# Optimization experiments

Hardware: AMD Instinct MI355X
Metric: run time of the kernel (lower is better)

The kernel has to match this reference:

```python
import jax, jax.numpy as jnp
import numpy as np

N = 100000      # nodes
E = 1600000     # edges
IN = 128        # in_dim
PE = 16         # pe_dim
HID = 128       # hid_dim
LAT = 64        # lat_dim
K = 4           # Chebyshev order


def setup_inputs() -> dict:
    key = jax.random.key(0)
    ks = jax.random.split(key, 12)
    f_in = IN + PE
    return {
        "x": jax.random.normal(ks[0], (N, IN), dtype=jnp.float32),
        "edge_index": jax.random.randint(ks[1], (2, E), 0, N, dtype=jnp.int32),
        "lap_pe": jax.random.normal(ks[2], (N, PE), dtype=jnp.float32),
        "edge_weight": jax.random.uniform(ks[3], (E,), dtype=jnp.float32),
        "W1": jax.random.normal(ks[4], (K, f_in, HID), dtype=jnp.float32) / np.sqrt(f_in),
        "b1": jnp.zeros((HID,), dtype=jnp.float32),
        "W2": jax.random.normal(ks[5], (K, HID, HID), dtype=jnp.float32) / np.sqrt(HID),
        "b2": jnp.zeros((HID,), dtype=jnp.float32),
        "W_mu": jax.random.normal(ks[6], (HID, LAT), dtype=jnp.float32) / np.sqrt(HID),
        "b_mu": jnp.zeros((LAT,), dtype=jnp.float32),
        "W_lv": jax.random.normal(ks[7], (HID, LAT), dtype=jnp.float32) / np.sqrt(HID),
        "b_lv": jnp.zeros((LAT,), dtype=jnp.float32),
    }


def _propagate(h, src, dst, w_hat):
    # (L_hat h)_i = sum_{(j->i)} w_hat_e * h_j   (one SpMM hop)
    return jax.ops.segment_sum(w_hat[:, None] * h[src], dst, num_segments=N)


def _cheb_conv(h, W, b, src, dst, w_hat):
    # PyG ChebConv recurrence: T0 = h, T1 = L_hat h, T_k = 2 L_hat T_{k-1} - T_{k-2}
    out = h @ W[0]
    tx0, tx1 = h, _propagate(h, src, dst, w_hat)
    out = out + tx1 @ W[1]
    for k in range(2, K):
        tx2 = 2.0 * _propagate(tx1, src, dst, w_hat) - tx0
        out = out + tx2 @ W[k]
        tx0, tx1 = tx1, tx2
    return out + b


def reference(x, edge_index, lap_pe, edge_weight, W1, b1, W2, b2, W_mu, b_mu, W_lv, b_lv):
    h = jnp.concatenate([x, lap_pe], axis=1)  # [N, IN+PE]
    src, dst = edge_index[0], edge_index[1]
    # ChebConv removes self loops before building the Laplacian -> zero their weight
    w = jnp.where(src == dst, 0.0, edge_weight)
    deg = jax.ops.segment_sum(w, src, num_segments=N)
    dinv = jnp.where(deg > 0, 1.0 / jnp.sqrt(deg), 0.0)
    # scaled Laplacian with lambda_max=2: L_hat = L - I = -D^{-1/2} A D^{-1/2}
    w_hat = -dinv[src] * w * dinv[dst]
    h = jax.nn.relu(_cheb_conv(h, W1, b1, src, dst, w_hat))
    h = jax.nn.relu(_cheb_conv(h, W2, b2, src, dst, w_hat))
    # scatter_mean with all-zero index == global mean pooling -> [1, HID]
    g = jnp.mean(h, axis=0, keepdims=True)
    return g @ W_mu + b_mu, g @ W_lv + b_lv
```

## Files before the change

### kernel.cpp

```cpp
#include <hip/hip_runtime.h>
#include <hip/hip_bf16.h>

#define IN_DIM 128
#define PE_DIM 16
#define F_IN 144
#define HID 128
#define LAT 64
#define K_CHEB 4

typedef unsigned int uint;
typedef unsigned short ushort;
typedef unsigned char uchar;
typedef __attribute__((ext_vector_type(8))) short short8;
typedef __attribute__((ext_vector_type(4))) float floatx4;
typedef __attribute__((ext_vector_type(2))) float floatx2;

__device__ __forceinline__ ushort f2bf(float f) {
    uint u = __float_as_uint(f);
    uint r = (u + 0x7FFFu + ((u >> 16) & 1u)) >> 16;
    return (ushort)r;
}
__device__ __forceinline__ uint bf_pack(float lo, float hi) {
    return (uint)f2bf(lo) | ((uint)f2bf(hi) << 16);
}

template<bool HI>
__device__ __forceinline__ floatx2 fp8x2_f32(uint v) {
    return __builtin_amdgcn_cvt_pk_f32_fp8((int)v, HI);
}
template<bool HI>
__device__ __forceinline__ uint f32_fp8x2(float a, float b, uint old) {
    return (uint)__builtin_amdgcn_cvt_pk_fp8_f32(a, b, (int)old, HI);
}

__global__ void zero_kernel(float* __restrict__ p, size_t n) {
    size_t i = (size_t)blockIdx.x * 256 + threadIdx.x;
    if (i < n) p[i] = 0.f;
}


__global__ __launch_bounds__(256) void bin_hist(const int* __restrict__ ei,
                                                int* __restrict__ ghA,
                                                int* __restrict__ ghB, int E) {
    __shared__ int hA[256], hB[256];
    int t = threadIdx.x;
    hA[t] = 0; hB[t] = 0;
    __syncthreads();
    int base = blockIdx.x * 4096;
#pragma unroll
    for (int j = 0; j < 16; j++) {
        int e = base + t + j * 256;
        if (e < E) {
            int s = ei[e], d = ei[E + e];
            atomicAdd(&hA[s >> 9], 1);
            atomicAdd(&hB[d >> 9], 1);
        }
    }
    __syncthreads();
    atomicAdd(&ghA[t], hA[t]);
    atomicAdd(&ghB[t], hB[t]);
}

__global__ __launch_bounds__(256) void bin_scan(const int* __restrict__ ghA,
                                                const int* __restrict__ ghB,
                                                int* __restrict__ bbA, int* __restrict__ curA,
                                                int* __restrict__ bbB, int* __restrict__ curB) {
    __shared__ int s[256];
    int t = threadIdx.x;
    int v = ghA[t];
    s[t] = v; __syncthreads();
    for (int off = 1; off < 256; off <<= 1) {
        int u = (t >= off) ? s[t - off] : 0;
        __syncthreads(); s[t] += u; __syncthreads();
    }
    bbA[t] = s[t] - v; curA[t] = s[t] - v;
    if (t == 255) bbA[256] = s[255];
    __syncthreads();
    int v2 = ghB[t];
    s[t] = v2; __syncthreads();
    for (int off = 1; off < 256; off <<= 1) {
        int u = (t >= off) ? s[t - off] : 0;
        __syncthreads(); s[t] += u; __syncthreads();
    }
    bbB[t] = s[t] - v2; curB[t] = s[t] - v2;
    if (t == 255) bbB[256] = s[255];
}

template<int BYDST>
__global__ __launch_bounds__(256) void bin_scatter(const int* __restrict__ ei,
                                                   const float* __restrict__ ew,
                                                   int* __restrict__ cursor,
                                                   uint2* __restrict__ outS, int E) {
    __shared__ uint2 rec[4096];
    __shared__ int pos[4096];
    __shared__ int hist[256], hscan[256], hrun[256], baseG[256];
    int t = threadIdx.x;
    hist[t] = 0;
    __syncthreads();
    int base = blockIdx.x * 4096;
    int cntBlk = E - base; if (cntBlk > 4096) cntBlk = 4096;
#pragma unroll
    for (int j = 0; j < 16; j++) {
        int e = base + t + j * 256;
        if (e < E) {
            int s = ei[e], d = ei[E + e];
            int key = BYDST ? d : s;
            atomicAdd(&hist[key >> 9], 1);
        }
    }
    __syncthreads();
    int v = hist[t];
    hscan[t] = v; __syncthreads();
    for (int off = 1; off < 256; off <<= 1) {
        int u = (t >= off) ? hscan[t - off] : 0;
        __syncthreads(); hscan[t] += u; __syncthreads();
    }
    int excl = hscan[t] - v;
    hscan[t] = excl;
    baseG[t] = atomicAdd(&cursor[t], v);
    hrun[t] = excl;
    __syncthreads();
#pragma unroll
    for (int j = 0; j < 16; j++) {
        int e = base + t + j * 256;
        if (e < E) {
            int s = ei[e], d = ei[E + e];
            float w = (s == d) ? 0.f : ew[e];
            int key = BYDST ? d : s;
            int b = key >> 9;
            int slot = atomicAdd(&hrun[b], 1);
            uint2 r;
            r.x = BYDST ? ((uint)s | ((uint)(d & 511) << 17)) : (uint)s;
            r.y = __float_as_uint(w);
            rec[slot] = r;
            pos[slot] = baseG[b] + (slot - hscan[b]);
        }
    }
    __syncthreads();
    for (int sI = t; sI < cntBlk; sI += 256) outS[pos[sI]] = rec[sI];
}

__global__ __launch_bounds__(256) void deg_bucket(const uint2* __restrict__ sA,
                                                  const int* __restrict__ bbA,
                                                  float* __restrict__ dinv, int N) {
    __shared__ float dl[512];
    int b = blockIdx.x, t = threadIdx.x;
    dl[t] = 0.f; dl[t + 256] = 0.f;
    __syncthreads();
    int s0 = bbA[b], s1 = bbA[b + 1];
    for (int r = s0 + t; r < s1; r += 256) {
        uint2 rc = sA[r];
        atomicAdd(&dl[(int)rc.x - (b << 9)], __uint_as_float(rc.y));
    }
    __syncthreads();
    for (int i = t; i < 512; i += 256) {
        int node = (b << 9) + i;
        if (node < N) {
            float d = dl[i];
            dinv[node] = (d > 0.f) ? rsqrtf(d) : 0.f;
        }
    }
}

__global__ __launch_bounds__(256) void csr_bucket(const uint2* __restrict__ sB,
                                                  const int* __restrict__ bbB,
                                                  const float* __restrict__ dinv,
                                                  int* __restrict__ rowp,
                                                  uint2* __restrict__ csr,
                                                  int N, int nbuck, int E) {
    __shared__ int cl[512], ol[512], orun[512];
    __shared__ float dvl[512];
    __shared__ int ps[256];
    int b = blockIdx.x, t = threadIdx.x;
    cl[t] = 0; cl[t + 256] = 0;
    for (int i = t; i < 512; i += 256) {
        int node = (b << 9) + i;
        dvl[i] = (node < N) ? dinv[node] : 0.f;
    }
    __syncthreads();
    int s0 = bbB[b], s1 = bbB[b + 1];
    for (int r = s0 + t; r < s1; r += 256)
        atomicAdd(&cl[(sB[r].x >> 17) & 511], 1);
    __syncthreads();
    int v0 = cl[2 * t], v1 = cl[2 * t + 1];
    int pv = v0 + v1;
    ps[t] = pv; __syncthreads();
    for (int off = 1; off < 256; off <<= 1) {
        int u = (t >= off) ? ps[t - off] : 0;
        __syncthreads(); ps[t] += u; __syncthreads();
    }
    int pexcl = ps[t] - pv;
    ol[2 * t] = pexcl;       ol[2 * t + 1] = pexcl + v0;
    orun[2 * t] = pexcl;     orun[2 * t + 1] = pexcl + v0;
    {
        int n0 = (b << 9) + 2 * t;
        if (n0 < N)     rowp[n0] = s0 + ol[2 * t];
        if (n0 + 1 < N) rowp[n0 + 1] = s0 + ol[2 * t + 1];
    }
    if (b == nbuck - 1 && t == 0) rowp[N] = E;
    __syncthreads();
    for (int r = s0 + t; r < s1; r += 256) {
        uint2 rc = sB[r];
        int src = rc.x & 0x1FFFF;
        int dl_ = (rc.x >> 17) & 511;
        float w = __uint_as_float(rc.y);
        int rank = atomicAdd(&orun[dl_], 1);
        float wh = -dinv[src] * w * dvl[dl_];
        uint2 o; o.x = (uint)src; o.y = __float_as_uint(wh);
        csr[s0 + rank] = o;
    }
}

__global__ void concat_x_fp8(const float* __restrict__ x, uint* __restrict__ T, size_t np) {
    size_t idx = (size_t)blockIdx.x * 256 + threadIdx.x;
    if (idx >= np) return;
    size_t i = idx >> 5; int p = (int)(idx & 31);
    float4 v = *(const float4*)(x + i * 128 + p * 4);
    uint o = f32_fp8x2<false>(v.x, v.y, 0u);
    o = f32_fp8x2<true>(v.z, v.w, o);
    T[i * 144 + p] = o;
}
__global__ void concat_pe_fp8(const float* __restrict__ pe, uint* __restrict__ T, size_t np) {
    size_t idx = (size_t)blockIdx.x * 256 + threadIdx.x;
    if (idx >= np) return;
    size_t i = idx >> 2; int p = (int)(idx & 3);
    float4 v = *(const float4*)(pe + i * 16 + p * 4);
    uint o = f32_fp8x2<false>(v.x, v.y, 0u);
    o = f32_fp8x2<true>(v.z, v.w, o);
    T[i * 144 + 32 + p] = o;
}

template<int K>
__global__ void wconv_kernel(const float* __restrict__ W, ushort* __restrict__ Bt) {
    int idx = blockIdx.x * 256 + threadIdx.x;
    if (idx >= 128 * K) return;
    int n = idx / K, kk = idx - n * K;
    Bt[idx] = f2bf(W[(size_t)kk * 128 + n]);
}

template<int F, int P>
__global__ __launch_bounds__(256) void prop_fp8(const uint* __restrict__ T,
                                                int off_src, int off_dst, int off_old,
                                                int recur,
                                                const int* __restrict__ rowp,
                                                const uint2* __restrict__ csrE, int n) {
    int node = blockIdx.x * 4 + (threadIdx.x >> 6);
    if (node >= n) return;
    int lane = threadIdx.x & 63;
    int g = lane >> 4;
    int ll = lane & 15;
    int e0 = rowp[node], e1 = rowp[node + 1];

    const uint* Tsrc = T + off_src;

    float acc[8];
#pragma unroll
    for (int i = 0; i < 8; i++) acc[i] = 0.f;
    float ex[4] = {0.f, 0.f, 0.f, 0.f};

    for (int base = e0; base < e1; base += 64) {
        int degc = e1 - base; if (degc > 64) degc = 64;
        int sidx = 0; float wval = 0.f;
        if (lane < degc) {
            uint2 rc = csrE[base + lane];
            sidx = (int)rc.x; wval = __uint_as_float(rc.y);
        }
        for (int j = 0; j < degc; j += 16) {
            int j0 = j + g, j1 = j0 + 4, j2 = j0 + 8, j3 = j0 + 12;
            int   s0 = __shfl(sidx, j0), s1 = __shfl(sidx, j1);
            int   s2 = __shfl(sidx, j2), s3 = __shfl(sidx, j3);
            float w0 = __shfl(wval, j0), w1 = __shfl(wval, j1);
            float w2 = __shfl(wval, j2), w3 = __shfl(wval, j3);
            const uint* hp0 = Tsrc + (size_t)s0 * P;
            const uint* hp1 = Tsrc + (size_t)s1 * P;
            const uint* hp2 = Tsrc + (size_t)s2 * P;
            const uint* hp3 = Tsrc + (size_t)s3 * P;
            uint2 v0 = *(const uint2*)(hp0 + ll * 2);
            uint2 v1 = *(const uint2*)(hp1 + ll * 2);
            uint2 v2 = *(const uint2*)(hp2 + ll * 2);
            uint2 v3 = *(const uint2*)(hp3 + ll * 2);
            uint x0 = 0, x1 = 0, x2 = 0, x3 = 0;
            if (F == 144) {
                if (ll < 4) {
                    x0 = hp0[32 + ll]; x1 = hp1[32 + ll];
                    x2 = hp2[32 + ll]; x3 = hp3[32 + ll];
                }
            }
#define ACC8(v, w) { \
            floatx2 f0 = fp8x2_f32<false>(v.x), f1 = fp8x2_f32<true>(v.x); \
            floatx2 f2 = fp8x2_f32<false>(v.y), f3 = fp8x2_f32<true>(v.y); \
            acc[0] += w * f0.x; acc[1] += w * f0.y; \
            acc[2] += w * f1.x; acc[3] += w * f1.y; \
            acc[4] += w * f2.x; acc[5] += w * f2.y; \
            acc[6] += w * f3.x; acc[7] += w * f3.y; }
            ACC8(v0, w0); ACC8(v1, w1); ACC8(v2, w2); ACC8(v3, w3);
#undef ACC8
            if (F == 144) {
                if (ll < 4) {
#define ACCX(xv, w) { \
                    floatx2 e0_ = fp8x2_f32<false>(xv), e1_ = fp8x2_f32<true>(xv); \
                    ex[0] += w * e0_.x; ex[1] += w * e0_.y; \
                    ex[2] += w * e1_.x; ex[3] += w * e1_.y; }
                    ACCX(x0, w0); ACCX(x1, w1); ACCX(x2, w2); ACCX(x3, w3);
#undef ACCX
                }
            }
        }
    }

#pragma unroll
    for (int i = 0; i < 8; i++) {
        acc[i] += __shfl_xor(acc[i], 16);
        acc[i] += __shfl_xor(acc[i], 32);
    }
    if (F == 144) {
#pragma unroll
        for (int i = 0; i < 4; i++) {
            ex[i] += __shfl_xor(ex[i], 16);
            ex[i] += __shfl_xor(ex[i], 32);
        }
    }

    if (g == 0) {
        uint* op = (uint*)T + off_dst + (size_t)node * P;
        const uint* tp = T + off_old + (size_t)node * P;
        if (recur) {
            uint2 ov = *(const uint2*)(tp + ll * 2);
            floatx2 f0 = fp8x2_f32<false>(ov.x), f1 = fp8x2_f32<true>(ov.x);
            floatx2 f2 = fp8x2_f32<false>(ov.y), f3 = fp8x2_f32<true>(ov.y);
            acc[0] = 2.f * acc[0] - f0.x; acc[1] = 2.f * acc[1] - f0.y;
            acc[2] = 2.f * acc[2] - f1.x; acc[3] = 2.f * acc[3] - f1.y;
            acc[4] = 2.f * acc[4] - f2.x; acc[5] = 2.f * acc[5] - f2.y;
            acc[6] = 2.f * acc[6] - f3.x; acc[7] = 2.f * acc[7] - f3.y;
            if (F == 144 && ll < 4) {
                uint ox = tp[32 + ll];
                floatx2 e0_ = fp8x2_f32<false>(ox), e1_ = fp8x2_f32<true>(ox);
                ex[0] = 2.f * ex[0] - e0_.x; ex[1] = 2.f * ex[1] - e0_.y;
                ex[2] = 2.f * ex[2] - e1_.x; ex[3] = 2.f * ex[3] - e1_.y;
            }
        }
        uint2 o;
        o.x = f32_fp8x2<false>(acc[0], acc[1], 0u);
        o.x = f32_fp8x2<true>(acc[2], acc[3], o.x);
        o.y = f32_fp8x2<false>(acc[4], acc[5], 0u);
        o.y = f32_fp8x2<true>(acc[6], acc[7], o.y);
        *(uint2*)(op + ll * 2) = o;
        if (F == 144 && ll < 4) {
            uint oe = f32_fp8x2<false>(ex[0], ex[1], 0u);
            oe = f32_fp8x2<true>(ex[2], ex[3], oe);
            op[32 + ll] = oe;
        }
    }
}

template<int K, bool REDUCE>
__global__ __launch_bounds__(256) void gemm_mfma(const uchar* __restrict__ A,
                                                 const ushort* __restrict__ Bt,
                                                 const float* __restrict__ bias,
                                                 uchar* __restrict__ Cb,
                                                 float* __restrict__ g,
                                                 int M, int CS) {
    __shared__ ushort As[64 * 40];
    __shared__ ushort Bs[128 * 40];
    __shared__ float colsum[128];
    int tid = threadIdx.x;
    int m0 = blockIdx.x * 64;
    int lane = tid & 63, wv = tid >> 6;
    int quad = lane >> 4, mrow = lane & 15;

    floatx4 acc[8];
#pragma unroll
    for (int c = 0; c < 8; c++) acc[c] = (floatx4){0.f, 0.f, 0.f, 0.f};
    if (REDUCE) { if (tid < 128) colsum[tid] = 0.f; }

    int ar = tid >> 2, ak = (tid & 3) * 8;
    int bn = tid >> 1, bk = (tid & 1) * 16;

    for (int k0 = 0; k0 < K; k0 += 32) {
        __syncthreads();
        uint2 av = make_uint2(0u, 0u);
        if (m0 + ar < M)
            av = *(const uint2*)(A + (size_t)(m0 + ar) * K + k0 + ak);
        floatx2 f0 = fp8x2_f32<false>(av.x), f1 = fp8x2_f32<true>(av.x);
        floatx2 f2 = fp8x2_f32<false>(av.y), f3 = fp8x2_f32<true>(av.y);
        uint4 pk;
        pk.x = bf_pack(f0.x, f0.y);
        pk.y = bf_pack(f1.x, f1.y);
        pk.z = bf_pack(f2.x, f2.y);
        pk.w = bf_pack(f3.x, f3.y);
        *(uint4*)(&As[ar * 40 + ak]) = pk;
        *(short8*)(&Bs[bn * 40 + bk]) = *(const short8*)(Bt + (size_t)bn * K + k0 + bk);
        *(short8*)(&Bs[bn * 40 + bk + 8]) = *(const short8*)(Bt + (size_t)bn * K + k0 + bk + 8);
        __syncthreads();
        short8 af = *(const short8*)(&As[(wv * 16 + mrow) * 40 + quad * 8]);
#pragma unroll
        for (int c = 0; c < 8; c++) {
            short8 bf = *(const short8*)(&Bs[(c * 16 + mrow) * 40 + quad * 8]);
            acc[c] = __builtin_amdgcn_mfma_f32_16x16x32_bf16(af, bf, acc[c], 0, 0, 0);
        }
    }

#pragma unroll
    for (int c = 0; c < 8; c++) {
        int col = c * 16 + mrow;
        float bsv = bias[col];
        if (REDUCE) {
            float part = 0.f;
#pragma unroll
            for (int r = 0; r < 4; r++) {
                int row = m0 + wv * 16 + quad * 4 + r;
                if (row < M) {
                    float v = acc[c][r] + bsv;
                    part += (v > 0.f) ? v : 0.f;
                }
            }
            part += __shfl_xor(part, 16);
            part += __shfl_xor(part, 32);
            if (quad == 0) atomicAdd(&colsum[col], part);
        } else {
#pragma unroll
            for (int r = 0; r < 4; r++) {
                int row = m0 + wv * 16 + quad * 4 + r;
                if (row < M) {
                    float v = acc[c][r] + bsv;
                    v = (v > 0.f) ? v : 0.f;
                    uint p = f32_fp8x2<false>(v, v, 0u);
                    Cb[(size_t)row * CS + col] = (uchar)(p & 0xFFu);
                }
            }
        }
    }
    if (REDUCE) {
        __syncthreads();
        if (tid < 128) atomicAdd(&g[tid], colsum[tid]);
    }
}

__global__ void head_kernel(const float* __restrict__ g,
                            const float* __restrict__ Wmu, const float* __restrict__ bmu,
                            const float* __restrict__ Wlv, const float* __restrict__ blv,
                            float* __restrict__ out, float invN) {
    __shared__ float gm[128];
    int tid = threadIdx.x;
    gm[tid] = g[tid] * invN;
    __syncthreads();
    if (tid < 64) {
        float acc = bmu[tid];
        for (int i = 0; i < 128; i++) acc += gm[i] * Wmu[i * 64 + tid];
        out[tid] = acc;
    } else {
        int j = tid - 64;
        float acc = blv[j];
        for (int i = 0; i < 128; i++) acc += gm[i] * Wlv[i * 64 + j];
        out[64 + j] = acc;
    }
}

static inline size_t align64(size_t x) { return (x + 63) & ~(size_t)63; }

extern "C" void kernel_launch(void* const* d_in, const int* in_sizes, int n_in,
                              void* d_out, int out_size, void* d_ws, size_t ws_size,
                              hipStream_t stream) {
    const float* x   = (const float*)d_in[0];
    const int*   ei  = (const int*)d_in[1];
    const float* pe  = (const float*)d_in[2];
    const float* ew  = (const float*)d_in[3];
    const float* W1  = (const float*)d_in[4];
    const float* b1  = (const float*)d_in[5];
    const float* W2  = (const float*)d_in[6];
    const float* b2  = (const float*)d_in[7];
    const float* Wmu = (const float*)d_in[8];
    const float* bmu = (const float*)d_in[9];
    const float* Wlv = (const float*)d_in[10];
    const float* blv = (const float*)d_in[11];
    float* out = (float*)d_out;

    const int N = in_sizes[0] / IN_DIM;
    const int E = in_sizes[3];
    const int NBUCK = (N + 511) >> 9;
    const int NBLK  = (E + 4095) / 4096;

    float* ws = (float*)d_ws;
    size_t o_g    = 0;
    size_t o_ghA  = o_g + 128;
    size_t o_ghB  = o_ghA + 256;
    size_t zeroLen = o_ghB + 256;
    size_t o_bbA  = align64(zeroLen);
    size_t o_curA = align64(o_bbA + 257);
    size_t o_bbB  = align64(o_curA + 256);
    size_t o_curB = align64(o_bbB + 257);
    size_t o_rowp = align64(o_curB + 256);
    size_t o_dinv = align64(o_rowp + N + 1);
    size_t o_sA   = align64(o_dinv + N);
    size_t o_sB   = align64(o_sA + 2 * (size_t)E);
    size_t o_csr  = align64(o_sB + 2 * (size_t)E);
    size_t o_Bt1  = align64(o_csr + 2 * (size_t)E);
    size_t o_Bt2  = align64(o_Bt1 + 128 * 576 / 2);
    size_t o_T1   = align64(o_Bt2 + 128 * 512 / 2);
    size_t o_T2   = align64(o_T1 + (size_t)N * 144);

    float* g     = ws + o_g;
    int*   ghA   = (int*)(ws + o_ghA);
    int*   ghB   = (int*)(ws + o_ghB);
    int*   bbA   = (int*)(ws + o_bbA);
    int*   curA  = (int*)(ws + o_curA);
    int*   bbB   = (int*)(ws + o_bbB);
    int*   curB  = (int*)(ws + o_curB);
    int*   rowp  = (int*)(ws + o_rowp);
    float* dinv  = ws + o_dinv;
    uint2* sA    = (uint2*)(ws + o_sA);
    uint2* sB    = (uint2*)(ws + o_sB);
    uint2* csr   = (uint2*)(ws + o_csr);
    ushort* Bt1  = (ushort*)(ws + o_Bt1);
    ushort* Bt2  = (ushort*)(ws + o_Bt2);
    uint*  T1    = (uint*)(ws + o_T1);
    uint*  T2    = (uint*)(ws + o_T2);

    dim3 b256(256);

    zero_kernel<<<dim3((unsigned)((zeroLen + 255) / 256)), b256, 0, stream>>>(ws, zeroLen);
    bin_hist<<<dim3(NBLK), b256, 0, stream>>>(ei, ghA, ghB, E);
    bin_scan<<<dim3(1), b256, 0, stream>>>(ghA, ghB, bbA, curA, bbB, curB);
    bin_scatter<0><<<dim3(NBLK), b256, 0, stream>>>(ei, ew, curA, sA, E);
    deg_bucket<<<dim3(NBUCK), b256, 0, stream>>>(sA, bbA, dinv, N);
    bin_scatter<1><<<dim3(NBLK), b256, 0, stream>>>(ei, ew, curB, sB, E);
    csr_bucket<<<dim3(NBUCK), b256, 0, stream>>>(sB, bbB, dinv, rowp, csr, N, NBUCK, E);

    wconv_kernel<576><<<dim3((128 * 576 + 255) / 256), b256, 0, stream>>>(W1, Bt1);
    wconv_kernel<512><<<dim3((128 * 512 + 255) / 256), b256, 0, stream>>>(W2, Bt2);

    concat_x_fp8<<<dim3((unsigned)(((size_t)N * 32 + 255) / 256)), b256, 0, stream>>>(x, T1, (size_t)N * 32);
    concat_pe_fp8<<<dim3((unsigned)(((size_t)N * 4 + 255) / 256)), b256, 0, stream>>>(pe, T1, (size_t)N * 4);

    const unsigned propGrid = (unsigned)((N + 3) / 4);
    const unsigned gemmGrid = (unsigned)((N + 63) / 64);

    prop_fp8<144, 144><<<propGrid, b256, 0, stream>>>(T1, 0,  36,  0,  0, rowp, csr, N);
    prop_fp8<144, 144><<<propGrid, b256, 0, stream>>>(T1, 36, 72,  0,  1, rowp, csr, N);
    prop_fp8<144, 144><<<propGrid, b256, 0, stream>>>(T1, 72, 108, 36, 1, rowp, csr, N);
    gemm_mfma<576, false><<<gemmGrid, b256, 0, stream>>>((const uchar*)T1, Bt1, b1, (uchar*)T2, g, N, 512);

    prop_fp8<128, 128><<<propGrid, b256, 0, stream>>>(T2, 0,  32, 0,  0, rowp, csr, N);
    prop_fp8<128, 128><<<propGrid, b256, 0, stream>>>(T2, 32, 64, 0,  1, rowp, csr, N);
    prop_fp8<128, 128><<<propGrid, b256, 0, stream>>>(T2, 64, 96, 32, 1, rowp, csr, N);
    gemm_mfma<512, true><<<gemmGrid, b256, 0, stream>>>((const uchar*)T2, Bt2, b2, (uchar*)nullptr, g, N, 0);

    head_kernel<<<dim3(1), dim3(128), 0, stream>>>(g, Wmu, bmu, Wlv, blv, out, 1.0f / (float)N);
}
```

Baseline: 672.4 us.

## Double GEMM M-tile to 128 rows and prefetch next K-slice into registers

The MFMA GEMM kernel now has each block cover 128 rows instead of 64. Each wave computes two 16-row fragments, so every B fragment read from shared memory feeds two MFMAs, and the grid is halved. Global loads for the next K-slice are issued into registers before the MFMAs of the current slice, which overlaps load latency with compute. The cost is more accumulator registers and twice the A-tile LDS, which may lower occupancy. Only the two GEMMs change, and the sparse propagation kernels, which dominate, are untouched.

```diff
diff --git a/kernel.cpp b/kernel.cpp
--- a/kernel.cpp
+++ b/kernel.cpp
@@ -360,44 +360,60 @@
                                                  uchar* __restrict__ Cb,
                                                  float* __restrict__ g,
                                                  int M, int CS) {
-    __shared__ ushort As[64 * 40];
+    __shared__ ushort As[128 * 40];
     __shared__ ushort Bs[128 * 40];
     __shared__ float colsum[128];
     int tid = threadIdx.x;
-    int m0 = blockIdx.x * 64;
+    int m0 = blockIdx.x * 128;
     int lane = tid & 63, wv = tid >> 6;
     int quad = lane >> 4, mrow = lane & 15;
 
-    floatx4 acc[8];
-#pragma unroll
-    for (int c = 0; c < 8; c++) acc[c] = (floatx4){0.f, 0.f, 0.f, 0.f};
+    floatx4 acc[2][8];
+#pragma unroll
+    for (int mf = 0; mf < 2; mf++)
+#pragma unroll
+        for (int c = 0; c < 8; c++) acc[mf][c] = (floatx4){0.f, 0.f, 0.f, 0.f};
     if (REDUCE) { if (tid < 128) colsum[tid] = 0.f; }
 
-    int ar = tid >> 2, ak = (tid & 3) * 8;
+    int ar = tid >> 1, ak = (tid & 1) * 16;
     int bn = tid >> 1, bk = (tid & 1) * 16;
 
+    uint4 aReg = make_uint4(0u, 0u, 0u, 0u);
+    if (m0 + ar < M) aReg = *(const uint4*)(A + (size_t)(m0 + ar) * K + ak);
+    short8 bReg0 = *(const short8*)(Bt + (size_t)bn * K + bk);
+    short8 bReg1 = *(const short8*)(Bt + (size_t)bn * K + bk + 8);
+
     for (int k0 = 0; k0 < K; k0 += 32) {
+        floatx2 f0 = fp8x2_f32<false>(aReg.x), f1 = fp8x2_f32<true>(aReg.x);
+        floatx2 f2 = fp8x2_f32<false>(aReg.y), f3 = fp8x2_f32<true>(aReg.y);
+        floatx2 f4 = fp8x2_f32<false>(aReg.z), f5 = fp8x2_f32<true>(aReg.z);
+        floatx2 f6 = fp8x2_f32<false>(aReg.w), f7 = fp8x2_f32<true>(aReg.w);
+        uint4 p0, p1;
+        p0.x = bf_pack(f0.x, f0.y); p0.y = bf_pack(f1.x, f1.y);
+        p0.z = bf_pack(f2.x, f2.y); p0.w = bf_pack(f3.x, f3.y);
+        p1.x = bf_pack(f4.x, f4.y); p1.y = bf_pack(f5.x, f5.y);
+        p1.z = bf_pack(f6.x, f6.y); p1.w = bf_pack(f7.x, f7.y);
+        *(uint4*)(&As[ar * 40 + ak]) = p0;
+        *(uint4*)(&As[ar * 40 + ak + 8]) = p1;
+        *(short8*)(&Bs[bn * 40 + bk]) = bReg0;
+        *(short8*)(&Bs[bn * 40 + bk + 8]) = bReg1;
         __syncthreads();
-        uint2 av = make_uint2(0u, 0u);
-        if (m0 + ar < M)
-            av = *(const uint2*)(A + (size_t)(m0 + ar) * K + k0 + ak);
-        floatx2 f0 = fp8x2_f32<false>(av.x), f1 = fp8x2_f32<true>(av.x);
-        floatx2 f2 = fp8x2_f32<false>(av.y), f3 = fp8x2_f32<true>(av.y);
-        uint4 pk;
-        pk.x = bf_pack(f0.x, f0.y);
-        pk.y = bf_pack(f1.x, f1.y);
-        pk.z = bf_pack(f2.x, f2.y);
-        pk.w = bf_pack(f3.x, f3.y);
-        *(uint4*)(&As[ar * 40 + ak]) = pk;
-        *(short8*)(&Bs[bn * 40 + bk]) = *(const short8*)(Bt + (size_t)bn * K + k0 + bk);
-        *(short8*)(&Bs[bn * 40 + bk + 8]) = *(const short8*)(Bt + (size_t)bn * K + k0 + bk + 8);
-        __syncthreads();
-        short8 af = *(const short8*)(&As[(wv * 16 + mrow) * 40 + quad * 8]);
+        int kn = k0 + 32;
+        if (kn < K) {
+            aReg = make_uint4(0u, 0u, 0u, 0u);
+            if (m0 + ar < M) aReg = *(const uint4*)(A + (size_t)(m0 + ar) * K + kn + ak);
+            bReg0 = *(const short8*)(Bt + (size_t)bn * K + kn + bk);
+            bReg1 = *(const short8*)(Bt + (size_t)bn * K + kn + bk + 8);
+        }
+        short8 af0 = *(const short8*)(&As[(wv * 32 + mrow) * 40 + quad * 8]);
+        short8 af1 = *(const short8*)(&As[(wv * 32 + 16 + mrow) * 40 + quad * 8]);
 #pragma unroll
         for (int c = 0; c < 8; c++) {
             short8 bf = *(const short8*)(&Bs[(c * 16 + mrow) * 40 + quad * 8]);
-            acc[c] = __builtin_amdgcn_mfma_f32_16x16x32_bf16(af, bf, acc[c], 0, 0, 0);
-        }
+            acc[0][c] = __builtin_amdgcn_mfma_f32_16x16x32_bf16(af0, bf, acc[0][c], 0, 0, 0);
+            acc[1][c] = __builtin_amdgcn_mfma_f32_16x16x32_bf16(af1, bf, acc[1][c], 0, 0, 0);
+        }
+        __syncthreads();
     }
 
 #pragma unroll
@@ -407,27 +423,31 @@
         if (REDUCE) {
             float part = 0.f;
 #pragma unroll
-            for (int r = 0; r < 4; r++) {
-                int row = m0 + wv * 16 + quad * 4 + r;
-                if (row < M) {
-                    float v = acc[c][r] + bsv;
-                    part += (v > 0.f) ? v : 0.f;
+            for (int mf = 0; mf < 2; mf++)
+#pragma unroll
+                for (int r = 0; r < 4; r++) {
+                    int row = m0 + wv * 32 + mf * 16 + quad * 4 + r;
+                    if (row < M) {
+                        float v = acc[mf][c][r] + bsv;
+                        part += (v > 0.f) ? v : 0.f;
+                    }
                 }
-            }
             part += __shfl_xor(part, 16);
             part += __shfl_xor(part, 32);
             if (quad == 0) atomicAdd(&colsum[col], part);
         } else {
 #pragma unroll
-            for (int r = 0; r < 4; r++) {
-                int row = m0 + wv * 16 + quad * 4 + r;
-                if (row < M) {
-                    float v = acc[c][r] + bsv;
-                    v = (v > 0.f) ? v : 0.f;
-                    uint p = f32_fp8x2<false>(v, v, 0u);
-                    Cb[(size_t)row * CS + col] = (uchar)(p & 0xFFu);
+            for (int mf = 0; mf < 2; mf++)
+#pragma unroll
+                for (int r = 0; r < 4; r++) {
+                    int row = m0 + wv * 32 + mf * 16 + quad * 4 + r;
+                    if (row < M) {
+                        float v = acc[mf][c][r] + bsv;
+                        v = (v > 0.f) ? v : 0.f;
+                        uint p = f32_fp8x2<false>(v, v, 0u);
+                        Cb[(size_t)row * CS + col] = (uchar)(p & 0xFFu);
+                    }
                 }
-            }
         }
     }
     if (REDUCE) {
@@ -533,7 +553,7 @@
     concat_pe_fp8<<<dim3((unsigned)(((size_t)N * 4 + 255) / 256)), b256, 0, stream>>>(pe, T1, (size_t)N * 4);
 
     const unsigned propGrid = (unsigned)((N + 3) / 4);
-    const unsigned gemmGrid = (unsigned)((N + 63) / 64);
+    const unsigned gemmGrid = (unsigned)((N + 127) / 128);
 
     prop_fp8<144, 144><<<propGrid, b256, 0, stream>>>(T1, 0,  36,  0,  0, rowp, csr, N);
     prop_fp8<144, 144><<<propGrid, b256, 0, stream>>>(T1, 36, 72,  0,  1, rowp, csr, N);
```

New measurement: 645.5 us. -4.0%, faster.
